# Optimization experiments

Hardware: AMD Instinct MI355X
Metric: run time of the kernel (lower is better)

Reference implementation:

```python
import jax, jax.numpy as jnp
import numpy as np

TOP_K = 2
LORA_SCALE = 32.0 / 16.0  # alpha / r


def setup_inputs() -> dict:
    key = jax.random.key(0)
    ks = jax.random.split(key, 11)
    B, S, H, I, E, R = 4, 2048, 2048, 5504, 8, 16
    s = lambda k, shape, fan: jax.random.normal(k, shape, jnp.float32) / np.sqrt(fan)
    return {
        "x": jax.random.normal(ks[0], (B, S, H), jnp.float32),
        "gate_values": jax.random.normal(ks[1], (B, E), jnp.float32),
        "Wg": s(ks[2], (I, H), H),
        "Ag": s(ks[3], (E, H, R), H),
        "Bg": s(ks[4], (E, R, I), R),
        "Wu": s(ks[5], (I, H), H),
        "Au": s(ks[6], (E, H, R), H),
        "Bu": s(ks[7], (E, R, I), R),
        "Wd": s(ks[8], (H, I), I),
        "Ad": s(ks[9], (E, I, R), I),
        "Bd": s(ks[10], (E, R, H), R),
    }


def _top_k_binary_gates(gate_values, k):
    # set top-k entries per row to 1.0, others 0.0 (bsz, num_experts)
    _, idx = jax.lax.top_k(gate_values, k)
    b = jnp.zeros_like(gate_values)
    rows = jnp.arange(gate_values.shape[0])[:, None]
    return b.at[rows, idx].set(1.0)


def _adapter_linear(x, W, A, B, binary_gates):
    # base: (b,s,in) @ (out,in)^T -> (b,s,out)
    base = jnp.einsum("bsh,oh->bso", x, W)
    # per-expert LoRA: gate e * x @ A_e @ B_e, summed over selected experts
    u = jnp.einsum("bsh,ehr->bser", x, A)            # (b,s,E,r) low-rank
    delta = jnp.einsum("bser,ero,be->bso", u, B, binary_gates)
    return base + LORA_SCALE * delta


def reference(x, gate_values, Wg, Ag, Bg, Wu, Au, Bu, Wd, Ad, Bd):
    g = _top_k_binary_gates(gate_values, TOP_K)
    gate_out = _adapter_linear(x, Wg, Ag, Bg, g)
    up_out = _adapter_linear(x, Wu, Au, Bu, g)
    h = jax.nn.silu(gate_out) * up_out              # SwiGLU
    return _adapter_linear(h, Wd, Ad, Bd, g)
```

## Files before the change

### kernel.cpp

```cpp
#include <hip/hip_runtime.h>
#include <stdint.h>

typedef unsigned short u16;
typedef __bf16 bf16x8 __attribute__((ext_vector_type(8)));
typedef float f32x4 __attribute__((ext_vector_type(4)));

#define AS1 __attribute__((address_space(1)))
#define AS3 __attribute__((address_space(3)))

__device__ __forceinline__ void g2l16(const void* g, void* l) {
  __builtin_amdgcn_global_load_lds((AS1 void*)(void*)g, (AS3 void*)l, 16, 0, 0);
}

__device__ __forceinline__ u16 f2bf(float f) {
  union { float f; uint32_t u; } v; v.f = f;
  return (u16)((v.u + 0x7fffu + ((v.u >> 16) & 1u)) >> 16);
}
__device__ __forceinline__ float bf2f(u16 b) {
  union { uint32_t u; float f; } v; v.u = ((uint32_t)b) << 16;
  return v.f;
}

__global__ void k_pre(const float* __restrict__ x, u16* __restrict__ xb,
                      const float* __restrict__ Wg, u16* __restrict__ Wgb,
                      const float* __restrict__ Wu, u16* __restrict__ Wub,
                      const float* __restrict__ Wd, u16* __restrict__ Wdb,
                      const float* __restrict__ gv,
                      const float* __restrict__ Ag, const float* __restrict__ Au,
                      const float* __restrict__ Ad,
                      const float* __restrict__ Bg, const float* __restrict__ Bu,
                      const float* __restrict__ Bd,
                      u16* __restrict__ AxT, u16* __restrict__ AdT,
                      u16* __restrict__ BgT, u16* __restrict__ BuT,
                      u16* __restrict__ BdT) {
  __shared__ int sidx[8];
  if (blockIdx.x < 49408) {
    int i = blockIdx.x * 256 + threadIdx.x;
    const float* in; u16* out; int j;
    if (i < 4194304) { in = x; out = xb; j = i; }
    else if (i < 4194304 + 2818048) { in = Wg; out = Wgb; j = i - 4194304; }
    else if (i < 4194304 + 2 * 2818048) { in = Wu; out = Wub; j = i - 4194304 - 2818048; }
    else { in = Wd; out = Wdb; j = i - 4194304 - 2 * 2818048; }
    float4 v = ((const float4*)in)[j];
    ushort4 o = make_ushort4(f2bf(v.x), f2bf(v.y), f2bf(v.z), f2bf(v.w));
    ((ushort4*)out)[j] = o;
    return;
  }
  if (threadIdx.x == 0) {
    #pragma unroll
    for (int b = 0; b < 4; ++b) {
      const float* g = gv + b * 8;
      int i1 = 0; float v1 = g[0];
      for (int e = 1; e < 8; ++e) if (g[e] > v1) { v1 = g[e]; i1 = e; }
      int i2 = -1; float v2 = -3.0e38f;
      for (int e = 0; e < 8; ++e) if (e != i1 && g[e] > v2) { v2 = g[e]; i2 = e; }
      sidx[2 * b] = i1; sidx[2 * b + 1] = i2;
    }
  }
  __syncthreads();
  int t = (blockIdx.x - 49408) * 256 + threadIdx.x;
  if (t < 524288) {
    int h = t % 2048;
    int j = (t / 2048) & 63;
    int b = t / (2048 * 64);
    const float* src = (j >= 32) ? Au : Ag;
    int jj = j & 31;
    int e = sidx[2 * b + ((jj >> 4) & 1)];
    AxT[t] = f2bf(src[((size_t)e * 2048 + h) * 16 + (jj & 15)]);
    return;
  }
  t -= 524288;
  if (t < 704512) {
    int h = t % 5504;
    int j = (t / 5504) & 31;
    int b = t / (5504 * 32);
    int e = sidx[2 * b + ((j >> 4) & 1)];
    AdT[t] = f2bf(Ad[((size_t)e * 5504 + h) * 16 + (j & 15)]);
    return;
  }
  t -= 704512;
  if (t < 704512) {
    int j = t & 31;
    int n = (t >> 5) % 5504;
    int b = t / (5504 * 32);
    int e = (j & 16) ? sidx[2 * b + 1] : sidx[2 * b];
    BgT[t] = f2bf(Bg[((size_t)e * 16 + (j & 15)) * 5504 + n]);
    return;
  }
  t -= 704512;
  if (t < 704512) {
    int j = t & 31;
    int n = (t >> 5) % 5504;
    int b = t / (5504 * 32);
    int e = (j & 16) ? sidx[2 * b + 1] : sidx[2 * b];
    BuT[t] = f2bf(Bu[((size_t)e * 16 + (j & 15)) * 5504 + n]);
    return;
  }
  t -= 704512;
  if (t < 262144) {
    int j = t & 31;
    int n = (t >> 5) % 2048;
    int b = t / (2048 * 32);
    int e = (j & 16) ? sidx[2 * b + 1] : sidx[2 * b];
    BdT[t] = f2bf(Bd[((size_t)e * 16 + (j & 15)) * 2048 + n]);
  }
}

template <int N2>
__global__ __launch_bounds__(256) void k_skinny(
    const u16* __restrict__ A, const u16* __restrict__ BT,
    float* __restrict__ part, int M, int K, int total_iters, int iters_per_chunk) {
  __shared__ u16 sA[128 * 64];
  __shared__ u16 sB[N2 * 64];
  int nm = M >> 7;
  int bm = blockIdx.x % nm, chunk = blockIdx.x / nm;
  int m0 = bm << 7;
  int batch = m0 >> 11;
  int tid = threadIdx.x, lane = tid & 63, w = tid >> 6;
  int kb = chunk * iters_per_chunk;
  int ke = min(total_iters, kb + iters_per_chunk);

  const u16* Bb = BT + (size_t)batch * N2 * K;

  const u16* ga[4]; u16* la[4];
  #pragma unroll
  for (int t = 0; t < 4; ++t) {
    int cb = 4 * w + t;
    int q = cb * 64 + lane;
    int row = q >> 3;
    int c = (q & 7) ^ (row & 7);
    ga[t] = A + (size_t)(m0 + row) * K + (size_t)kb * 64 + c * 8;
    la[t] = sA + cb * 512;
  }
  constexpr int nB = N2 / 32;
  const u16* gb[nB]; u16* lb[nB];
  #pragma unroll
  for (int t = 0; t < nB; ++t) {
    int cb = nB * w + t;
    int q = cb * 64 + lane;
    int row = q >> 3;
    int c = (q & 7) ^ (row & 7);
    gb[t] = Bb + (size_t)row * K + (size_t)kb * 64 + c * 8;
    lb[t] = sB + cb * 512;
  }

  f32x4 acc[2][N2 / 16] = {};
  for (int kt = kb; kt < ke; ++kt) {
    #pragma unroll
    for (int t = 0; t < 4; ++t) { g2l16(ga[t], la[t]); ga[t] += 64; }
    #pragma unroll
    for (int t = 0; t < nB; ++t) { g2l16(gb[t], lb[t]); gb[t] += 64; }
    __syncthreads();
    #pragma unroll
    for (int ks = 0; ks < 2; ++ks) {
      int cb0 = ks * 4 + (lane >> 4);
      bf16x8 af[2], bfr[N2 / 16];
      #pragma unroll
      for (int mi = 0; mi < 2; ++mi) {
        int row = 32 * w + mi * 16 + (lane & 15);
        af[mi] = *(const bf16x8*)(sA + (row * 8 + (cb0 ^ (row & 7))) * 8);
      }
      #pragma unroll
      for (int ni = 0; ni < N2 / 16; ++ni) {
        int row = ni * 16 + (lane & 15);
        bfr[ni] = *(const bf16x8*)(sB + (row * 8 + (cb0 ^ (row & 7))) * 8);
      }
      #pragma unroll
      for (int mi = 0; mi < 2; ++mi)
        #pragma unroll
        for (int ni = 0; ni < N2 / 16; ++ni)
          acc[mi][ni] = __builtin_amdgcn_mfma_f32_16x16x32_bf16(
              af[mi], bfr[ni], acc[mi][ni], 0, 0, 0);
    }
    __syncthreads();
  }

  int rb = (lane >> 4) * 4, cc = lane & 15;
  #pragma unroll
  for (int mi = 0; mi < 2; ++mi)
    #pragma unroll
    for (int ni = 0; ni < N2 / 16; ++ni)
      #pragma unroll
      for (int reg = 0; reg < 4; ++reg) {
        int gr = m0 + 32 * w + mi * 16 + rb + reg;
        int gc = ni * 16 + cc;
        part[((size_t)chunk * M + gr) * N2 + gc] = acc[mi][ni][reg];
      }
}

__global__ void k_fin(const float* __restrict__ part, u16* __restrict__ out0,
                      u16* __restrict__ out1, int M, int N2, int nch) {
  int t = blockIdx.x * 256 + threadIdx.x;
  if (t >= M * N2) return;
  float s = 0.f;
  for (int c = 0; c < nch; ++c) s += part[(size_t)c * M * N2 + t];
  int j = t % N2, bs = t / N2;
  u16 v = f2bf(2.0f * s);
  if (N2 == 64) {
    if (j < 32) out0[(size_t)bs * 32 + j] = v;
    else        out1[(size_t)bs * 32 + (j - 32)] = v;
  } else {
    out0[(size_t)bs * 32 + j] = v;
  }
}

__global__ void k_haf(const float* __restrict__ haf, u16* __restrict__ ha) {
  int t = blockIdx.x * 256 + threadIdx.x;
  if (t < 262144) ha[t] = f2bf(2.0f * haf[t]);
}

__global__ __launch_bounds__(256, 2)
void k_gemmGU(const u16* __restrict__ A, const u16* __restrict__ Bg_,
              const u16* __restrict__ Bu_,
              const u16* __restrict__ A2g, const u16* __restrict__ A2u,
              const u16* __restrict__ B2g, const u16* __restrict__ B2u,
              const u16* __restrict__ AdT, float* __restrict__ haf,
              u16* __restrict__ Out, int N, int K) {
  __shared__ u16 sA[128 * 64];
  __shared__ u16 sG[128 * 64];
  __shared__ u16 sU[128 * 64];
  int nt = N >> 7;
  int nm = gridDim.x / nt;
  int perx = nm >> 3;
  int xcd = blockIdx.x & 7;
  int v = blockIdx.x >> 3;
  int bn = v / perx;
  int bm = xcd * perx + (v - bn * perx);
  int m0 = bm << 7, n0 = bn << 7;
  int batch = m0 >> 11;
  int tid = threadIdx.x, lane = tid & 63, w = tid >> 6;
  int mo = (w & 1) << 6, no = (w >> 1) << 6;

  const u16* ga[4]; const u16* gg[4]; const u16* gu[4];
  u16* la[4]; u16* lg[4]; u16* lu[4];
  #pragma unroll
  for (int t = 0; t < 4; ++t) {
    int cb = 4 * w + t;
    int q = cb * 64 + lane;
    int row = q >> 3;
    int c = (q & 7) ^ (row & 7);
    ga[t] = A + (size_t)(m0 + row) * K + c * 8;
    gg[t] = Bg_ + (size_t)(n0 + row) * K + c * 8;
    gu[t] = Bu_ + (size_t)(n0 + row) * K + c * 8;
    la[t] = sA + cb * 512;
    lg[t] = sG + cb * 512;
    lu[t] = sU + cb * 512;
  }

  f32x4 accg[4][4] = {};
  f32x4 accu[4][4] = {};

  int kiters = K >> 6;
  for (int kt = 0; kt < kiters; ++kt) {
    #pragma unroll
    for (int t = 0; t < 4; ++t) { g2l16(ga[t], la[t]); ga[t] += 64; }
    #pragma unroll
    for (int t = 0; t < 4; ++t) { g2l16(gg[t], lg[t]); gg[t] += 64; }
    #pragma unroll
    for (int t = 0; t < 4; ++t) { g2l16(gu[t], lu[t]); gu[t] += 64; }
    __syncthreads();
    #pragma unroll
    for (int ks = 0; ks < 2; ++ks) {
      bf16x8 af[4], bgf[4], buf_[4];
      int cb0 = ks * 4 + (lane >> 4);
      #pragma unroll
      for (int mi = 0; mi < 4; ++mi) {
        int row = mo + mi * 16 + (lane & 15);
        af[mi] = *(const bf16x8*)(sA + (row * 8 + (cb0 ^ (row & 7))) * 8);
      }
      #pragma unroll
      for (int ni = 0; ni < 4; ++ni) {
        int row = no + ni * 16 + (lane & 15);
        bgf[ni] = *(const bf16x8*)(sG + (row * 8 + (cb0 ^ (row & 7))) * 8);
        buf_[ni] = *(const bf16x8*)(sU + (row * 8 + (cb0 ^ (row & 7))) * 8);
      }
      #pragma unroll
      for (int mi = 0; mi < 4; ++mi)
        #pragma unroll
        for (int ni = 0; ni < 4; ++ni) {
          accg[mi][ni] = __builtin_amdgcn_mfma_f32_16x16x32_bf16(
              af[mi], bgf[ni], accg[mi][ni], 0, 0, 0);
          accu[mi][ni] = __builtin_amdgcn_mfma_f32_16x16x32_bf16(
              af[mi], buf_[ni], accu[mi][ni], 0, 0, 0);
        }
    }
    __syncthreads();
  }

  {
    const u16* B2gb = B2g + (size_t)batch * N * 32;
    const u16* B2ub = B2u + (size_t)batch * N * 32;
    #pragma unroll
    for (int t = 0; t < 2; ++t) {
      int cb = 2 * w + t;
      int q = cb * 64 + lane;
      int row = q >> 2;
      int c = (q & 3) ^ (row & 3);
      g2l16(A2g + (size_t)(m0 + row) * 32 + c * 8, sA + cb * 512);
      g2l16(A2u + (size_t)(m0 + row) * 32 + c * 8, sA + 4096 + cb * 512);
      g2l16(B2gb + (size_t)(n0 + row) * 32 + c * 8, sG + cb * 512);
      g2l16(B2ub + (size_t)(n0 + row) * 32 + c * 8, sU + cb * 512);
    }
    __syncthreads();
    int c0 = lane >> 4;
    bf16x8 ag2[4], au2[4], bg2[4], bu2[4];
    #pragma unroll
    for (int mi = 0; mi < 4; ++mi) {
      int row = mo + mi * 16 + (lane & 15);
      ag2[mi] = *(const bf16x8*)(sA + (row * 4 + (c0 ^ (row & 3))) * 8);
      au2[mi] = *(const bf16x8*)(sA + 4096 + (row * 4 + (c0 ^ (row & 3))) * 8);
    }
    #pragma unroll
    for (int ni = 0; ni < 4; ++ni) {
      int row = no + ni * 16 + (lane & 15);
      bg2[ni] = *(const bf16x8*)(sG + (row * 4 + (c0 ^ (row & 3))) * 8);
      bu2[ni] = *(const bf16x8*)(sU + (row * 4 + (c0 ^ (row & 3))) * 8);
    }
    #pragma unroll
    for (int mi = 0; mi < 4; ++mi)
      #pragma unroll
      for (int ni = 0; ni < 4; ++ni) {
        accg[mi][ni] = __builtin_amdgcn_mfma_f32_16x16x32_bf16(
            ag2[mi], bg2[ni], accg[mi][ni], 0, 0, 0);
        accu[mi][ni] = __builtin_amdgcn_mfma_f32_16x16x32_bf16(
            au2[mi], bu2[ni], accu[mi][ni], 0, 0, 0);
      }
  }

  __syncthreads();

  {
    const u16* AdTb = AdT + (size_t)batch * 32 * 5504;
    int q = w * 64 + lane;
    int row = q >> 3;
    int c = (q & 7) ^ (row & 7);
    #pragma unroll
    for (int half = 0; half < 2; ++half)
      g2l16(AdTb + (size_t)row * 5504 + n0 + half * 64 + c * 8,
            sA + half * 2048 + w * 512);
  }

  int rb = (lane >> 4) * 4;
  int cc = lane & 15;
  #pragma unroll
  for (int mi = 0; mi < 4; ++mi) {
    #pragma unroll
    for (int ni = 0; ni < 4; ++ni) {
      #pragma unroll
      for (int reg = 0; reg < 4; ++reg) {
        int gr = m0 + mo + mi * 16 + rb + reg;
        int gc = n0 + no + ni * 16 + cc;
        size_t pos = (size_t)gr * N + gc;
        float gvv = accg[mi][ni][reg];
        float uvv = accu[mi][ni][reg];
        gvv = gvv / (1.f + __expf(-gvv));
        u16 hv = f2bf(gvv * uvv);
        Out[pos] = hv;
        int cl = no + ni * 16 + cc;
        u16* sH = (cl < 64) ? sG : sU;
        int c2 = cl & 63;
        int r2 = mo + mi * 16 + rb + reg;
        sH[(r2 * 8 + ((c2 >> 3) ^ (r2 & 7))) * 8 + (c2 & 7)] = hv;
      }
    }
  }
  __syncthreads();

  {
    int moh = (w & 1) << 6;
    int half = w >> 1;
    const u16* sH = half ? sU : sG;
    const u16* sAd = sA + half * 2048;
    f32x4 ah[4][2] = {};
    #pragma unroll
    for (int ks = 0; ks < 2; ++ks) {
      int cb0 = ks * 4 + (lane >> 4);
      bf16x8 afh[4], bfh[2];
      #pragma unroll
      for (int mi = 0; mi < 4; ++mi) {
        int row = moh + mi * 16 + (lane & 15);
        afh[mi] = *(const bf16x8*)(sH + (row * 8 + (cb0 ^ (row & 7))) * 8);
      }
      #pragma unroll
      for (int jf = 0; jf < 2; ++jf) {
        int row = jf * 16 + (lane & 15);
        bfh[jf] = *(const bf16x8*)(sAd + (row * 8 + (cb0 ^ (row & 7))) * 8);
      }
      #pragma unroll
      for (int mi = 0; mi < 4; ++mi)
        #pragma unroll
        for (int jf = 0; jf < 2; ++jf)
          ah[mi][jf] = __builtin_amdgcn_mfma_f32_16x16x32_bf16(
              afh[mi], bfh[jf], ah[mi][jf], 0, 0, 0);
    }
    #pragma unroll
    for (int mi = 0; mi < 4; ++mi)
      #pragma unroll
      for (int jf = 0; jf < 2; ++jf)
        #pragma unroll
        for (int reg = 0; reg < 4; ++reg)
          atomicAdd(haf + (size_t)(m0 + moh + mi * 16 + rb + reg) * 32 +
                        jf * 16 + cc,
                    ah[mi][jf][reg]);
  }
}

__global__ __launch_bounds__(256, 2)
void k_gemmD(const u16* __restrict__ A, const u16* __restrict__ Bm,
             const u16* __restrict__ A2, const u16* __restrict__ B2,
             float* __restrict__ Out, int N, int K) {
  __shared__ u16 sA0[128 * 64];
  __shared__ u16 sA1[128 * 64];
  __shared__ u16 sB[128 * 64];
  int nt = N >> 7;
  int nm = gridDim.x / nt;
  int perx = nm >> 3;
  int xcd = blockIdx.x & 7;
  int v = blockIdx.x >> 3;
  int bn = v / perx;
  int bm = xcd * perx + (v - bn * perx);
  int m0 = bm << 8, n0 = bn << 7;
  int batch = m0 >> 11;
  int tid = threadIdx.x, lane = tid & 63, w = tid >> 6;
  int mo = (w & 1) << 6, no = (w >> 1) << 6;

  const u16* ga0[4]; const u16* ga1[4]; const u16* gb[4];
  u16* la0[4]; u16* la1[4]; u16* lb[4];
  #pragma unroll
  for (int t = 0; t < 4; ++t) {
    int cb = 4 * w + t;
    int q = cb * 64 + lane;
    int row = q >> 3;
    int c = (q & 7) ^ (row & 7);
    ga0[t] = A + (size_t)(m0 + row) * K + c * 8;
    ga1[t] = A + (size_t)(m0 + 128 + row) * K + c * 8;
    gb[t]  = Bm + (size_t)(n0 + row) * K + c * 8;
    la0[t] = sA0 + cb * 512;
    la1[t] = sA1 + cb * 512;
    lb[t]  = sB + cb * 512;
  }

  f32x4 acc0[4][4] = {};
  f32x4 acc1[4][4] = {};

  int kiters = K >> 6;
  for (int kt = 0; kt < kiters; ++kt) {
    #pragma unroll
    for (int t = 0; t < 4; ++t) { g2l16(ga0[t], la0[t]); ga0[t] += 64; }
    #pragma unroll
    for (int t = 0; t < 4; ++t) { g2l16(ga1[t], la1[t]); ga1[t] += 64; }
    #pragma unroll
    for (int t = 0; t < 4; ++t) { g2l16(gb[t], lb[t]); gb[t] += 64; }
    __syncthreads();
    #pragma unroll
    for (int ks = 0; ks < 2; ++ks) {
      bf16x8 af0[4], af1[4], bfr[4];
      int cb0 = ks * 4 + (lane >> 4);
      #pragma unroll
      for (int mi = 0; mi < 4; ++mi) {
        int row = mo + mi * 16 + (lane & 15);
        af0[mi] = *(const bf16x8*)(sA0 + (row * 8 + (cb0 ^ (row & 7))) * 8);
        af1[mi] = *(const bf16x8*)(sA1 + (row * 8 + (cb0 ^ (row & 7))) * 8);
      }
      #pragma unroll
      for (int ni = 0; ni < 4; ++ni) {
        int row = no + ni * 16 + (lane & 15);
        bfr[ni] = *(const bf16x8*)(sB + (row * 8 + (cb0 ^ (row & 7))) * 8);
      }
      #pragma unroll
      for (int mi = 0; mi < 4; ++mi)
        #pragma unroll
        for (int ni = 0; ni < 4; ++ni) {
          acc0[mi][ni] = __builtin_amdgcn_mfma_f32_16x16x32_bf16(
              af0[mi], bfr[ni], acc0[mi][ni], 0, 0, 0);
          acc1[mi][ni] = __builtin_amdgcn_mfma_f32_16x16x32_bf16(
              af1[mi], bfr[ni], acc1[mi][ni], 0, 0, 0);
        }
    }
    __syncthreads();
  }

  {
    const u16* B2b = B2 + (size_t)batch * N * 32;
    #pragma unroll
    for (int t = 0; t < 2; ++t) {
      int cb = 2 * w + t;
      int q = cb * 64 + lane;
      int row = q >> 2;
      int c = (q & 3) ^ (row & 3);
      g2l16(A2 + (size_t)(m0 + row) * 32 + c * 8, sA0 + cb * 512);
      g2l16(A2 + (size_t)(m0 + 128 + row) * 32 + c * 8, sA1 + cb * 512);
      g2l16(B2b + (size_t)(n0 + row) * 32 + c * 8, sB + cb * 512);
    }
    __syncthreads();
    int c0 = lane >> 4;
    bf16x8 af0[4], af1[4], bfr[4];
    #pragma unroll
    for (int mi = 0; mi < 4; ++mi) {
      int row = mo + mi * 16 + (lane & 15);
      af0[mi] = *(const bf16x8*)(sA0 + (row * 4 + (c0 ^ (row & 3))) * 8);
      af1[mi] = *(const bf16x8*)(sA1 + (row * 4 + (c0 ^ (row & 3))) * 8);
    }
    #pragma unroll
    for (int ni = 0; ni < 4; ++ni) {
      int row = no + ni * 16 + (lane & 15);
      bfr[ni] = *(const bf16x8*)(sB + (row * 4 + (c0 ^ (row & 3))) * 8);
    }
    #pragma unroll
    for (int mi = 0; mi < 4; ++mi)
      #pragma unroll
      for (int ni = 0; ni < 4; ++ni) {
        acc0[mi][ni] = __builtin_amdgcn_mfma_f32_16x16x32_bf16(
            af0[mi], bfr[ni], acc0[mi][ni], 0, 0, 0);
        acc1[mi][ni] = __builtin_amdgcn_mfma_f32_16x16x32_bf16(
            af1[mi], bfr[ni], acc1[mi][ni], 0, 0, 0);
      }
  }

  int rb = (lane >> 4) * 4;
  int cc = lane & 15;
  #pragma unroll
  for (int mi = 0; mi < 4; ++mi) {
    #pragma unroll
    for (int ni = 0; ni < 4; ++ni) {
      #pragma unroll
      for (int reg = 0; reg < 4; ++reg) {
        int gr = m0 + mo + mi * 16 + rb + reg;
        int gc = n0 + no + ni * 16 + cc;
        Out[(size_t)gr * N + gc] = acc0[mi][ni][reg];
        Out[(size_t)(gr + 128) * N + gc] = acc1[mi][ni][reg];
      }
    }
  }
}

extern "C" void kernel_launch(void* const* d_in, const int* in_sizes, int n_in,
                              void* d_out, int out_size, void* d_ws, size_t ws_size,
                              hipStream_t stream) {
  const float* x  = (const float*)d_in[0];
  const float* gv = (const float*)d_in[1];
  const float* Wg = (const float*)d_in[2];
  const float* Ag = (const float*)d_in[3];
  const float* Bg = (const float*)d_in[4];
  const float* Wu = (const float*)d_in[5];
  const float* Au = (const float*)d_in[6];
  const float* Bu = (const float*)d_in[7];
  const float* Wd = (const float*)d_in[8];
  const float* Ad = (const float*)d_in[9];
  const float* Bd = (const float*)d_in[10];
  float* out = (float*)d_out;

  char* ws = (char*)d_ws;
  size_t off = 0;
  auto alloc = [&](size_t bytes) -> void* {
    void* p = ws + off;
    off = (off + bytes + 255) & ~(size_t)255;
    return p;
  };
  u16* xb   = (u16*)alloc((size_t)8192 * 2048 * 2);
  u16* Wgb  = (u16*)alloc((size_t)5504 * 2048 * 2);
  u16* Wub  = (u16*)alloc((size_t)5504 * 2048 * 2);
  u16* Wdb  = (u16*)alloc((size_t)2048 * 5504 * 2);
  u16* xag  = (u16*)alloc((size_t)8192 * 32 * 2);
  u16* xau  = (u16*)alloc((size_t)8192 * 32 * 2);
  u16* ha   = (u16*)alloc((size_t)8192 * 32 * 2);
  u16* BgT  = (u16*)alloc((size_t)4 * 5504 * 32 * 2);
  u16* BuT  = (u16*)alloc((size_t)4 * 5504 * 32 * 2);
  u16* BdT  = (u16*)alloc((size_t)4 * 2048 * 32 * 2);
  u16* AxT  = (u16*)alloc((size_t)4 * 64 * 2048 * 2);
  u16* AdT  = (u16*)alloc((size_t)4 * 32 * 5504 * 2);
  float* haf = (float*)alloc((size_t)8192 * 32 * 4);
  u16* gbuf = (u16*)alloc((size_t)8192 * 5504 * 2);
  if (off > ws_size) return;

  float* part_xa = (float*)gbuf;

  hipMemsetAsync(haf, 0, (size_t)8192 * 32 * 4, stream);

  k_pre<<<60736, 256, 0, stream>>>(x, xb, Wg, Wgb, Wu, Wub, Wd, Wdb,
                                   gv, Ag, Au, Ad, Bg, Bu, Bd,
                                   AxT, AdT, BgT, BuT, BdT);

  k_skinny<64><<<64 * 16, 256, 0, stream>>>(xb, AxT, part_xa, 8192, 2048, 32, 2);
  k_fin<<<2048, 256, 0, stream>>>(part_xa, xag, xau, 8192, 64, 16);

  k_gemmGU<<<64 * 43, 256, 0, stream>>>(xb, Wgb, Wub, xag, xau, BgT, BuT,
                                        AdT, haf, gbuf, 5504, 2048);

  k_haf<<<1024, 256, 0, stream>>>(haf, ha);

  k_gemmD<<<32 * 16, 256, 0, stream>>>(gbuf, Wdb, ha, BdT, out, 2048, 5504);
}
```

Before: 785.8 us.

## Unfuse down-proj LoRA A-projection from gate/up GEMM into separate skinny kernel

Removes the fused h·Ad low-rank projection, with its fp32 atomicAdd accumulation, from the gate/up GEMM epilogue. Instead, the existing skinny GEMM kernel followed by a reduction kernel computes it from the stored h buffer, reusing the Wg workspace for partials. This drops the extra LDS traffic, syncs and atomics from the big GEMM and may lower its register pressure. The cost is an extra read of the full h matrix plus two more kernel launches.

```diff
diff --git a/kernel.cpp b/kernel.cpp
--- a/kernel.cpp
+++ b/kernel.cpp
@@ -204,17 +204,11 @@
   }
 }
 
-__global__ void k_haf(const float* __restrict__ haf, u16* __restrict__ ha) {
-  int t = blockIdx.x * 256 + threadIdx.x;
-  if (t < 262144) ha[t] = f2bf(2.0f * haf[t]);
-}
-
 __global__ __launch_bounds__(256, 2)
 void k_gemmGU(const u16* __restrict__ A, const u16* __restrict__ Bg_,
               const u16* __restrict__ Bu_,
               const u16* __restrict__ A2g, const u16* __restrict__ A2u,
               const u16* __restrict__ B2g, const u16* __restrict__ B2u,
-              const u16* __restrict__ AdT, float* __restrict__ haf,
               u16* __restrict__ Out, int N, int K) {
   __shared__ u16 sA[128 * 64];
   __shared__ u16 sG[128 * 64];
@@ -327,19 +321,6 @@
       }
   }
 
-  __syncthreads();
-
-  {
-    const u16* AdTb = AdT + (size_t)batch * 32 * 5504;
-    int q = w * 64 + lane;
-    int row = q >> 3;
-    int c = (q & 7) ^ (row & 7);
-    #pragma unroll
-    for (int half = 0; half < 2; ++half)
-      g2l16(AdTb + (size_t)row * 5504 + n0 + half * 64 + c * 8,
-            sA + half * 2048 + w * 512);
-  }
-
   int rb = (lane >> 4) * 4;
   int cc = lane & 15;
   #pragma unroll
@@ -354,54 +335,9 @@
         float gvv = accg[mi][ni][reg];
         float uvv = accu[mi][ni][reg];
         gvv = gvv / (1.f + __expf(-gvv));
-        u16 hv = f2bf(gvv * uvv);
-        Out[pos] = hv;
-        int cl = no + ni * 16 + cc;
-        u16* sH = (cl < 64) ? sG : sU;
-        int c2 = cl & 63;
-        int r2 = mo + mi * 16 + rb + reg;
-        sH[(r2 * 8 + ((c2 >> 3) ^ (r2 & 7))) * 8 + (c2 & 7)] = hv;
-      }
-    }
-  }
-  __syncthreads();
-
-  {
-    int moh = (w & 1) << 6;
-    int half = w >> 1;
-    const u16* sH = half ? sU : sG;
-    const u16* sAd = sA + half * 2048;
-    f32x4 ah[4][2] = {};
-    #pragma unroll
-    for (int ks = 0; ks < 2; ++ks) {
-      int cb0 = ks * 4 + (lane >> 4);
-      bf16x8 afh[4], bfh[2];
-      #pragma unroll
-      for (int mi = 0; mi < 4; ++mi) {
-        int row = moh + mi * 16 + (lane & 15);
-        afh[mi] = *(const bf16x8*)(sH + (row * 8 + (cb0 ^ (row & 7))) * 8);
-      }
-      #pragma unroll
-      for (int jf = 0; jf < 2; ++jf) {
-        int row = jf * 16 + (lane & 15);
-        bfh[jf] = *(const bf16x8*)(sAd + (row * 8 + (cb0 ^ (row & 7))) * 8);
-      }
-      #pragma unroll
-      for (int mi = 0; mi < 4; ++mi)
-        #pragma unroll
-        for (int jf = 0; jf < 2; ++jf)
-          ah[mi][jf] = __builtin_amdgcn_mfma_f32_16x16x32_bf16(
-              afh[mi], bfh[jf], ah[mi][jf], 0, 0, 0);
-    }
-    #pragma unroll
-    for (int mi = 0; mi < 4; ++mi)
-      #pragma unroll
-      for (int jf = 0; jf < 2; ++jf)
-        #pragma unroll
-        for (int reg = 0; reg < 4; ++reg)
-          atomicAdd(haf + (size_t)(m0 + moh + mi * 16 + rb + reg) * 32 +
-                        jf * 16 + cc,
-                    ah[mi][jf][reg]);
+        Out[pos] = f2bf(gvv * uvv);
+      }
+    }
   }
 }
 
@@ -569,13 +505,11 @@
   u16* BdT  = (u16*)alloc((size_t)4 * 2048 * 32 * 2);
   u16* AxT  = (u16*)alloc((size_t)4 * 64 * 2048 * 2);
   u16* AdT  = (u16*)alloc((size_t)4 * 32 * 5504 * 2);
-  float* haf = (float*)alloc((size_t)8192 * 32 * 4);
   u16* gbuf = (u16*)alloc((size_t)8192 * 5504 * 2);
   if (off > ws_size) return;
 
   float* part_xa = (float*)gbuf;
-
-  hipMemsetAsync(haf, 0, (size_t)8192 * 32 * 4, stream);
+  float* part_ha = (float*)Wgb;
 
   k_pre<<<60736, 256, 0, stream>>>(x, xb, Wg, Wgb, Wu, Wub, Wd, Wdb,
                                    gv, Ag, Au, Ad, Bg, Bu, Bd,
@@ -585,9 +519,10 @@
   k_fin<<<2048, 256, 0, stream>>>(part_xa, xag, xau, 8192, 64, 16);
 
   k_gemmGU<<<64 * 43, 256, 0, stream>>>(xb, Wgb, Wub, xag, xau, BgT, BuT,
-                                        AdT, haf, gbuf, 5504, 2048);
-
-  k_haf<<<1024, 256, 0, stream>>>(haf, ha);
+                                        gbuf, 5504, 2048);
+
+  k_skinny<32><<<64 * 16, 256, 0, stream>>>(gbuf, AdT, part_ha, 8192, 5504, 86, 6);
+  k_fin<<<1024, 256, 0, stream>>>(part_ha, ha, ha, 8192, 32, 16);
 
   k_gemmD<<<32 * 16, 256, 0, stream>>>(gbuf, Wdb, ha, BdT, out, 2048, 5504);
 }
```

New measurement: 801.7 us. 2.0% more time.
